# Optimization experiments

Hardware: AMD Instinct MI355X
Metric: run time of the kernel (lower is better)

Reference implementation:

```python
import jax, jax.numpy as jnp
import numpy as np

V = 4
H, W, Z = 32, 64, 13
C = 256
NH = 8
WS = (4, 4, 1)
SS = (2, 2, 0)
HID = 1024


def _layernorm(x, g, b):
    mu = jnp.mean(x, axis=-1, keepdims=True)
    var = jnp.mean((x - mu) ** 2, axis=-1, keepdims=True)
    return (x - mu) * jax.lax.rsqrt(var + 1e-5) * g + b


def setup_inputs() -> dict:
    key = jax.random.key(0)
    ks = jax.random.split(key, 12)
    B = 2
    s = 0.02
    return {
        "x_z": jax.random.normal(ks[0], (B, H, W, Z, C), jnp.float32),
        "x_q": jax.random.normal(ks[1], (B, H, W, Z, C), jnp.float32),
        "x_t": jax.random.normal(ks[2], (B, H, W, Z, C), jnp.float32),
        "x_u": jax.random.normal(ks[3], (B, H, W, Z, C), jnp.float32),
        "qkv_w": jax.random.normal(ks[4], (V, C, 3 * C), jnp.float32) * s,
        "qkv_b": jnp.zeros((V, 3 * C), jnp.float32),
        "proj_w": jax.random.normal(ks[5], (V, C, C), jnp.float32) * s,
        "proj_b": jnp.zeros((V, C), jnp.float32),
        "n1_g": jnp.ones((V, C), jnp.float32),
        "n1_b": jnp.zeros((V, C), jnp.float32),
        "n2_g": jnp.ones((V, C), jnp.float32),
        "n2_b": jnp.zeros((V, C), jnp.float32),
        "fc1_w": jax.random.normal(ks[6], (V, C, HID), jnp.float32) * s,
        "fc1_b": jnp.zeros((V, HID), jnp.float32),
        "fc2_w": jax.random.normal(ks[7], (V, HID, C), jnp.float32) * s,
        "fc2_b": jnp.zeros((V, C), jnp.float32),
    }


def reference(x_z, x_q, x_t, x_u, qkv_w, qkv_b, proj_w, proj_b,
              n1_g, n1_b, n2_g, n2_b, fc1_w, fc1_b, fc2_w, fc2_b):
    x = jnp.stack([x_z, x_q, x_t, x_u], axis=0)  # [V,B,H,W,Z,C]
    B = x.shape[1]
    L = H * W * Z
    w0, w1, w2 = WS
    N = w0 * w1 * w2
    hd = C // NH
    scale = hd ** -0.5

    shortcut = x.reshape(V, B, L, C)
    xn = _layernorm(shortcut, n1_g[:, None, None, :], n1_b[:, None, None, :])
    xs = xn.reshape(V, B, H, W, Z, C)
    # cyclic shift (same sign used for both rolls in the source)
    xs = jnp.roll(xs, shift=SS, axis=(2, 3, 4))
    # window partition -> [V, B_, N, C]
    xw = xs.reshape(V, B, H // w0, w0, W // w1, w1, Z // w2, w2, C)
    xw = xw.transpose(0, 1, 2, 4, 6, 3, 5, 7, 8).reshape(V, -1, N, C)
    B_ = xw.shape[1]

    qkv = jnp.einsum('vbnc,vcd->vbnd', xw, qkv_w) + qkv_b[:, None, None, :]
    qkv = qkv.reshape(V, B_, N, 3, NH, hd).transpose(3, 1, 0, 4, 2, 5)  # [3,B_,V,NH,N,hd]
    q, k, v = qkv[0], qkv[1], qkv[2]
    # per-(variable, head) attention: heads of different variables are concatenated
    attn = jax.nn.softmax(jnp.einsum('bvhnd,bvhmd->bvhnm', q * scale, k), axis=-1)
    ctx = jnp.einsum('bvhnm,bvhmd->bvhnd', attn, v)  # [B_,V,NH,N,hd]
    # faithful to torch reshape (B_, N, V*NH, hd) -> (B_, V*N, C): rows interleave (n, v)
    big = ctx.transpose(0, 3, 1, 2, 4).reshape(B_, V * N, C)
    y = big.reshape(B_, V, N, C).transpose(1, 0, 2, 3)  # slice [:, i*N:(i+1)*N]
    y = jnp.einsum('vbnc,vcd->vbnd', y, proj_w) + proj_b[:, None, None, :]
    # window reverse
    y = y.reshape(V, B, H // w0, W // w1, Z // w2, w0, w1, w2, C)
    y = y.transpose(0, 1, 2, 5, 3, 6, 4, 7, 8).reshape(V, B, H, W, Z, C)
    y = jnp.roll(y, shift=SS, axis=(2, 3, 4))  # same-sign roll (preserves source behavior)
    y = y.reshape(V, B, L, C)

    x2 = shortcut + y
    xm = _layernorm(x2, n2_g[:, None, None, :], n2_b[:, None, None, :])
    h = jax.nn.gelu(jnp.einsum('vblc,vcd->vbld', xm, fc1_w) + fc1_b[:, None, None, :],
                    approximate=False)
    m = jnp.einsum('vbld,vdc->vblc', h, fc2_w) + fc2_b[:, None, None, :]
    out = (x2 + m).reshape(V, B, H, W, Z, C)
    return out  # stacked per-variable outputs in variable_order
```

## Files before the change

kernel.cpp:

```cpp
#include <hip/hip_runtime.h>
#include <hip/hip_bf16.h>
#include <cstdint>
#include <cstddef>

#define DI __device__ __forceinline__

typedef __bf16 bf16_t;
typedef bf16_t bf16x8 __attribute__((ext_vector_type(8)));
typedef float f32x4 __attribute__((ext_vector_type(4)));

constexpr int Vn = 4, Bn = 2, Hn = 32, Wn = 64, Zn = 13, Cn = 256, HIDn = 1024;
constexpr int Ln = Hn * Wn * Zn;
constexpr int BWn = Bn * (Hn / 4) * (Wn / 4) * Zn;
constexpr int PB = Bn * Ln;
constexpr int ROWS = Vn * PB;

DI void gload_lds16(const void* g, void* l) {
  __builtin_amdgcn_global_load_lds(
      (const __attribute__((address_space(1))) void*)g,
      (__attribute__((address_space(3))) void*)l, 16, 0, 0);
}

DI unsigned short f2bf_bits(float f) {
  __hip_bfloat16 h = __float2bfloat16(f);
  return *reinterpret_cast<unsigned short*>(&h);
}

DI float gelu_f(float x) {
  float u = x * x;
  float w = x * fmaf(0.044715f, u, 1.0f);
  float e = __expf(-1.5957691216057308f * w);
  return x * __builtin_amdgcn_rcpf(1.0f + e);
}

__global__ __launch_bounds__(256) void transpose_tile_kernel(
    const float* __restrict__ src, __hip_bfloat16* __restrict__ dst, int K, int N) {
  __shared__ float S[64][65];
  const int n0 = blockIdx.x * 64, k0 = blockIdx.y * 64, v = blockIdx.z;
  const int tc = threadIdx.x & 63, tr = threadIdx.x >> 6;
#pragma unroll
  for (int i = 0; i < 16; ++i) {
    int kk = tr + i * 4;
    S[kk][tc] = src[((size_t)v * K + k0 + kk) * N + n0 + tc];
  }
  __syncthreads();
#pragma unroll
  for (int i = 0; i < 16; ++i) {
    int nn = tr + i * 4;
    dst[((size_t)v * N + n0 + nn) * K + k0 + tc] = __float2bfloat16(S[tc][nn]);
  }
}

__global__ __launch_bounds__(256) void ln1_kernel(
    const float* __restrict__ x0, const float* __restrict__ x1,
    const float* __restrict__ x2i, const float* __restrict__ x3,
    const float* __restrict__ g_, const float* __restrict__ b_,
    __hip_bfloat16* __restrict__ xw) {
  int gw = blockIdx.x * 4 + (threadIdx.x >> 6);
  int lane = threadIdx.x & 63;
  int v = gw / PB;
  int rem = gw - v * PB;
  int bw = rem >> 4, nn = rem & 15;
  int zb = bw % 13;
  int t = bw / 13;
  int wb = t & 15, t2 = t >> 4;
  int hb = t2 & 7, b = t2 >> 3;
  int hs = (hb * 4 + (nn >> 2) + 30) & 31;
  int wsrc = (wb * 4 + (nn & 3) + 62) & 63;
  size_t l = (size_t)(hs * 64 + wsrc) * 13 + zb;
  const float* xv = (v == 0) ? x0 : (v == 1) ? x1 : (v == 2) ? x2i : x3;
  const float* xp = xv + ((size_t)b * Ln + l) * 256;
  float4 val = *(const float4*)(xp + lane * 4);
  float s = val.x + val.y + val.z + val.w;
  float sq = val.x * val.x + val.y * val.y + val.z * val.z + val.w * val.w;
#pragma unroll
  for (int o = 32; o; o >>= 1) {
    s += __shfl_xor(s, o);
    sq += __shfl_xor(sq, o);
  }
  float mean = s * (1.0f / 256.0f);
  float var = sq * (1.0f / 256.0f) - mean * mean;
  float rstd = rsqrtf(var + 1e-5f);
  const float* gg = g_ + v * 256 + lane * 4;
  const float* bb = b_ + v * 256 + lane * 4;
  ushort4 o4;
  o4.x = f2bf_bits((val.x - mean) * rstd * gg[0] + bb[0]);
  o4.y = f2bf_bits((val.y - mean) * rstd * gg[1] + bb[1]);
  o4.z = f2bf_bits((val.z - mean) * rstd * gg[2] + bb[2]);
  o4.w = f2bf_bits((val.w - mean) * rstd * gg[3] + bb[3]);
  *reinterpret_cast<ushort4*>(xw + (size_t)gw * 256 + lane * 4) = o4;
}

__global__ __launch_bounds__(256) void attn_kernel(
    const __hip_bfloat16* __restrict__ qkvp, __hip_bfloat16* __restrict__ ctx) {
  __shared__ float P[4][16][17];
  int b_ = blockIdx.x;
  int v = blockIdx.y;
  int wid = threadIdx.x >> 6, lane = threadIdx.x & 63;
  int lm = lane & 15, hi = lane >> 4;
  const bf16_t* base = (const bf16_t*)qkvp + (size_t)(v * BWn + b_) * 16 * 768;
  const float scale = 0.17677669529663687f;
  f32x4 zero = {0.f, 0.f, 0.f, 0.f};
#pragma unroll
  for (int hh = 0; hh < 2; ++hh) {
    int h = wid + 4 * hh;
    bf16x8 qf = *(const bf16x8*)(base + (size_t)lm * 768 + h * 32 + hi * 8);
    bf16x8 kf = *(const bf16x8*)(base + (size_t)lm * 768 + 256 + h * 32 + hi * 8);
    f32x4 s = __builtin_amdgcn_mfma_f32_16x16x32_bf16(qf, kf, zero, 0, 0, 0);
    float p0[4];
#pragma unroll
    for (int q = 0; q < 4; ++q) {
      float val = s[q] * scale;
      float mx = val;
#pragma unroll
      for (int o = 8; o >= 1; o >>= 1) mx = fmaxf(mx, __shfl_xor(mx, o));
      float e = __expf(val - mx);
      float sum = e;
#pragma unroll
      for (int o = 8; o >= 1; o >>= 1) sum += __shfl_xor(sum, o);
      p0[q] = e * __builtin_amdgcn_rcpf(sum);
    }
#pragma unroll
    for (int q = 0; q < 4; ++q) P[wid][hi * 4 + q][lm] = p0[q];
    bf16x8 pa;
#pragma unroll
    for (int j = 0; j < 8; ++j) pa[j] = (bf16_t)0.f;
    if (hi < 2) {
#pragma unroll
      for (int j = 0; j < 8; ++j) pa[j] = (bf16_t)P[wid][lm][hi * 8 + j];
    }
#pragma unroll
    for (int dh = 0; dh < 2; ++dh) {
      bf16x8 vf;
#pragma unroll
      for (int j = 0; j < 8; ++j) vf[j] = (bf16_t)0.f;
      if (hi < 2) {
#pragma unroll
        for (int j = 0; j < 8; ++j)
          vf[j] = base[(size_t)(hi * 8 + j) * 768 + 512 + h * 32 + dh * 16 + lm];
      }
      f32x4 c = __builtin_amdgcn_mfma_f32_16x16x32_bf16(pa, vf, zero, 0, 0, 0);
#pragma unroll
      for (int q = 0; q < 4; ++q) {
        int n = hi * 4 + q;
        int d = dh * 16 + lm;
        int r = n * 4 + v;
        int vo = r >> 4, no = r & 15;
        ctx[((size_t)(vo * BWn + b_) * 16 + no) * 256 + h * 32 + d] = __float2bfloat16(c[q]);
      }
    }
  }
}

template <int EPI, int K, int N>
__global__ __launch_bounds__(256, 3) void gemm4(
    const __hip_bfloat16* __restrict__ A, const __hip_bfloat16* __restrict__ WT,
    const float* __restrict__ bias, __hip_bfloat16* __restrict__ outb,
    float* __restrict__ outf, const float* __restrict__ xi0,
    const float* __restrict__ xi1, const float* __restrict__ xi2,
    const float* __restrict__ xi3) {
  constexpr int NT = K / 64;
  constexpr int NC = N / 128;
  const int v = blockIdx.z;
  const int x = blockIdx.x;
  const int xcd = x & 7;
  const int j = x >> 3;
  const int c = j % NC;
  const int r = xcd + 8 * (j / NC);
  const int rowBase = r * 128;
  const int colBase = c * 128;

  const bf16_t* Av = (const bf16_t*)A + ((size_t)v * PB + rowBase) * K;
  const bf16_t* Wv = (const bf16_t*)WT + ((size_t)v * N + colBase) * K;

  __shared__ __align__(16) uint8_t smem[40960];
  bf16_t(*As)[64] = (bf16_t(*)[64])smem;
  bf16_t(*Bs)[64] = (bf16_t(*)[64])(smem + 16384);

  const int tid = threadIdx.x, wid = tid >> 6, lane = tid & 63;
  const int wr = wid >> 1, wc = wid & 1;
  const int lm = lane & 15, hi = lane >> 4;
  const int rA = lane >> 3;
  const int lg = (lane & 7) ^ rA;

  f32x4 acc[4][4];
#pragma unroll
  for (int m = 0; m < 4; ++m)
#pragma unroll
    for (int n = 0; n < 4; ++n) acc[m][n] = f32x4{0.f, 0.f, 0.f, 0.f};

  for (int t = 0; t < NT; ++t) {
    if (t) __syncthreads();
#pragma unroll
    for (int g = 0; g < 4; ++g) {
      int grp = wid * 4 + g;
      gload_lds16(Av + (size_t)(grp * 8 + rA) * K + t * 64 + lg * 8, &As[grp * 8][0]);
    }
#pragma unroll
    for (int g = 0; g < 4; ++g) {
      int grp = wid * 4 + g;
      gload_lds16(Wv + (size_t)(grp * 8 + rA) * K + t * 64 + lg * 8, &Bs[grp * 8][0]);
    }
    __syncthreads();
#pragma unroll
    for (int kk = 0; kk < 2; ++kk) {
      bf16x8 af[4], bfv[4];
#pragma unroll
      for (int m = 0; m < 4; ++m) {
        const int rr = wr * 64 + m * 16 + lm;
        af[m] = *(const bf16x8*)&As[rr][((kk * 4 + hi) ^ (lm & 7)) * 8];
      }
#pragma unroll
      for (int n = 0; n < 4; ++n) {
        const int rr = wc * 64 + n * 16 + lm;
        bfv[n] = *(const bf16x8*)&Bs[rr][((kk * 4 + hi) ^ (lm & 7)) * 8];
      }
#pragma unroll
      for (int m = 0; m < 4; ++m)
#pragma unroll
        for (int n = 0; n < 4; ++n)
          acc[m][n] = __builtin_amdgcn_mfma_f32_16x16x32_bf16(af[m], bfv[n], acc[m][n], 0, 0, 0);
    }
  }

  __syncthreads();
  uint8_t* ep = smem + wid * 10240;

  if constexpr (EPI == 0) {
    ushort(*E)[72] = (ushort(*)[72])ep;
    float bcol[4];
#pragma unroll
    for (int n = 0; n < 4; ++n) bcol[n] = bias[v * N + colBase + wc * 64 + n * 16 + lm];
#pragma unroll
    for (int m = 0; m < 4; ++m)
#pragma unroll
      for (int q = 0; q < 4; ++q) {
        int lr = m * 16 + hi * 4 + q;
#pragma unroll
        for (int n = 0; n < 4; ++n) E[lr][n * 16 + lm] = f2bf_bits(acc[m][n][q] + bcol[n]);
      }
    const int pr = lane >> 3, pc = lane & 7;
#pragma unroll
    for (int p = 0; p < 8; ++p) {
      int lr = p * 8 + pr;
      bf16x8 val = *(const bf16x8*)&E[lr][pc * 8];
      size_t grow = (size_t)v * PB + rowBase + wr * 64 + lr;
      int gcol = colBase + wc * 64 + pc * 8;
      *(bf16x8*)&outb[grow * N + gcol] = val;
    }
  } else {
    float(*F)[36] = (float(*)[36])ep;
    const int pr = lane >> 3, pc = lane & 7;
#pragma unroll
    for (int h2 = 0; h2 < 2; ++h2) {
#pragma unroll
      for (int m = 0; m < 4; ++m)
#pragma unroll
        for (int q = 0; q < 4; ++q) {
          int lr = m * 16 + hi * 4 + q;
#pragma unroll
          for (int n2 = 0; n2 < 2; ++n2) F[lr][n2 * 16 + lm] = acc[m][h2 * 2 + n2][q];
        }
#pragma unroll
      for (int p = 0; p < 8; ++p) {
        int lr = p * 8 + pr;
        f32x4 a4 = *(const f32x4*)&F[lr][pc * 4];
        int rowv = rowBase + wr * 64 + lr;
        int gcol = colBase + wc * 64 + h2 * 32 + pc * 4;
        f32x4 b4 = *(const f32x4*)&bias[v * N + gcol];
        int b_ = rowv >> 4, nn = rowv & 15;
        int zb = b_ % 13;
        int tt = b_ / 13;
        int wb = tt & 15, tt2 = tt >> 4;
        int hb = tt2 & 7, bb = tt2 >> 3;
        int h2v = (hb * 4 + (nn >> 2) + 2) & 31;
        int w2v = (wb * 4 + (nn & 3) + 2) & 63;
        size_t l = (size_t)(h2v * 64 + w2v) * 13 + zb;
        const float* xv = (v == 0) ? xi0 : (v == 1) ? xi1 : (v == 2) ? xi2 : xi3;
        f32x4 x4 = *(const f32x4*)(xv + ((size_t)bb * Ln + l) * 256 + gcol);
        f32x4 o4 = a4 + b4 + x4;
        *(f32x4*)(outf + (((size_t)v * Bn + bb) * Ln + l) * 256 + gcol) = o4;
      }
      if (h2 == 0) __builtin_amdgcn_s_waitcnt(0);
    }
  }
}

__global__ __launch_bounds__(512, 4) void mlp_fused6(
    const float* __restrict__ x2,
    const __hip_bfloat16* __restrict__ W1T,
    const __hip_bfloat16* __restrict__ W2T,
    const float* __restrict__ b1, const float* __restrict__ b2,
    const float* __restrict__ g2, const float* __restrict__ bt2,
    float* __restrict__ outp) {
  const int v = blockIdx.z;
  const size_t gRow0 = (size_t)v * PB + (size_t)blockIdx.x * 128;

  __shared__ __align__(16) uint8_t smem[73728];
  uint8_t* hb = smem + 65536;

  const int tid = threadIdx.x, wid = tid >> 6, lane = tid & 63;
  const int lm = lane & 15, hi = lane >> 4;
  const int rA = lane >> 3, lg = (lane & 7) ^ rA;

  {
    f32x4 g4 = *(const f32x4*)(g2 + v * 256 + lane * 4);
    f32x4 b4l = *(const f32x4*)(bt2 + v * 256 + lane * 4);
    for (int i = 0; i < 16; ++i) {
      int r = wid * 16 + i;
      const float* xp = x2 + (gRow0 + r) * 256;
      float4 val = *(const float4*)(xp + lane * 4);
      float s = val.x + val.y + val.z + val.w;
      float sq = val.x * val.x + val.y * val.y + val.z * val.z + val.w * val.w;
#pragma unroll
      for (int o = 32; o; o >>= 1) {
        s += __shfl_xor(s, o);
        sq += __shfl_xor(sq, o);
      }
      float mean = s * (1.0f / 256.0f);
      float var = sq * (1.0f / 256.0f) - mean * mean;
      float rstd = rsqrtf(var + 1e-5f);
      ushort4 o4;
      o4.x = f2bf_bits((val.x - mean) * rstd * g4[0] + b4l[0]);
      o4.y = f2bf_bits((val.y - mean) * rstd * g4[1] + b4l[1]);
      o4.z = f2bf_bits((val.z - mean) * rstd * g4[2] + b4l[2]);
      o4.w = f2bf_bits((val.w - mean) * rstd * g4[3] + b4l[3]);
      int gph = ((lm >> 1) ^ (r & 7) ^ hi) & 7;
      *(ushort4*)(smem + hi * 16384 + r * 128 + gph * 16 + (lm & 1) * 8) = o4;
    }
  }
  __syncthreads();

  bf16x8 xnf[4][2];
  {
    int r = wid * 16 + lm;
#pragma unroll
    for (int t = 0; t < 4; ++t)
#pragma unroll
      for (int kk = 0; kk < 2; ++kk) {
        int gph = ((kk * 4 + hi) ^ (r & 7) ^ t) & 7;
        xnf[t][kk] = *(const bf16x8*)(smem + t * 16384 + r * 128 + gph * 16);
      }
  }

  f32x4 acc2[16];
#pragma unroll
  for (int ca = 0; ca < 16; ++ca) acc2[ca] = f32x4{0.f, 0.f, 0.f, 0.f};

  const bf16_t* W1v = (const bf16_t*)W1T + (size_t)v * 1024 * 256;
  const bf16_t* W2v = (const bf16_t*)W2T + (size_t)v * 256 * 1024;

  auto stageW = [&](uint8_t* W1c, uint8_t* W2c, int hc) {
#pragma unroll
    for (int s = 0; s < 2; ++s) {
      int idx = wid * 2 + s;
      int t = idx >> 2, grp = idx & 3;
      gload_lds16(W1v + (size_t)(hc * 32 + grp * 8 + rA) * 256 + t * 64 + lg * 8,
                  W1c + t * 4096 + grp * 1024);
    }
#pragma unroll
    for (int s = 0; s < 2; ++s) {
      int i = wid * 2 + s;
      int p = i * 8 + rA;
      int col = 2 * p + (lg >> 2);
      gload_lds16(W2v + (size_t)col * 1024 + hc * 32 + (lg & 3) * 8, W2c + i * 1024);
    }
  };

  __syncthreads();
  stageW(smem, smem + 16384, 0);
  __syncthreads();

  for (int hc = 0; hc < 32; ++hc) {
    const int cur = hc & 1;
    uint8_t* W1c = smem + (cur ? 32768 : 0);
    uint8_t* W2c = smem + (cur ? 49152 : 16384);
    if (hc + 1 < 32)
      stageW(smem + (cur ? 0 : 32768), smem + (cur ? 16384 : 49152), hc + 1);

    int xr = wid * 16 + lm;
    int p = xr >> 1;
#pragma unroll
    for (int t2 = 0; t2 < 2; ++t2) {
      f32x4 acc1 = f32x4{0.f, 0.f, 0.f, 0.f};
      int hw = t2 * 16 + lm;
#pragma unroll
      for (int t = 0; t < 4; ++t)
#pragma unroll
        for (int kk = 0; kk < 2; ++kk) {
          bf16x8 w1f = *(const bf16x8*)(W1c + t * 4096 + hw * 128 +
                                        (((kk * 4 + hi) ^ (hw & 7)) & 7) * 16);
          acc1 = __builtin_amdgcn_mfma_f32_16x16x32_bf16(w1f, xnf[t][kk], acc1, 0, 0, 0);
        }
      f32x4 b1v = *(const f32x4*)&b1[v * 1024 + hc * 32 + t2 * 16 + hi * 4];
      ushort4 hp;
      hp.x = f2bf_bits(gelu_f(acc1[0] + b1v[0]));
      hp.y = f2bf_bits(gelu_f(acc1[1] + b1v[1]));
      hp.z = f2bf_bits(gelu_f(acc1[2] + b1v[2]));
      hp.w = f2bf_bits(gelu_f(acc1[3] + b1v[3]));
      int glog = (xr & 1) * 4 + t2 * 2 + (hi >> 1);
      int gph = (glog ^ (p & 7)) & 7;
      *(ushort4*)(hb + p * 128 + gph * 16 + (hi & 1) * 8) = hp;
    }
    __syncthreads();

    {
      bf16x8 hf = *(const bf16x8*)(hb + p * 128 + ((((xr & 1) * 4 + hi) ^ (p & 7)) & 7) * 16);
#pragma unroll
      for (int ca = 0; ca < 16; ++ca) {
        int col = ca * 16 + lm;
        int p2 = col >> 1;
        bf16x8 w2f = *(const bf16x8*)(W2c + p2 * 128 +
                                      ((((col & 1) * 4 + hi) ^ (p2 & 7)) & 7) * 16);
        acc2[ca] = __builtin_amdgcn_mfma_f32_16x16x32_bf16(w2f, hf, acc2[ca], 0, 0, 0);
      }
    }
    __syncthreads();
  }

  {
    size_t orow = gRow0 + wid * 16 + lm;
    float* obase = outp + orow * 256;
#pragma unroll
    for (int ca = 0; ca < 16; ++ca) {
      int col = ca * 16 + hi * 4;
      f32x4 b4 = *(const f32x4*)&b2[v * 256 + col];
      float* o = obase + col;
      f32x4 cur = *(const f32x4*)o;
      f32x4 res = cur + acc2[ca] + b4;
      *(f32x4*)o = res;
    }
  }
}

extern "C" void kernel_launch(void* const* d_in, const int* in_sizes, int n_in,
                              void* d_out, int out_size, void* d_ws, size_t ws_size,
                              hipStream_t stream) {
  const float* x0 = (const float*)d_in[0];
  const float* x1 = (const float*)d_in[1];
  const float* x2i = (const float*)d_in[2];
  const float* x3 = (const float*)d_in[3];
  const float* qkv_w = (const float*)d_in[4];
  const float* qkv_b = (const float*)d_in[5];
  const float* proj_w = (const float*)d_in[6];
  const float* proj_b = (const float*)d_in[7];
  const float* n1g = (const float*)d_in[8];
  const float* n1b = (const float*)d_in[9];
  const float* n2g = (const float*)d_in[10];
  const float* n2b = (const float*)d_in[11];
  const float* fc1_w = (const float*)d_in[12];
  const float* fc1_b = (const float*)d_in[13];
  const float* fc2_w = (const float*)d_in[14];
  const float* fc2_b = (const float*)d_in[15];
  float* out = (float*)d_out;

  uint8_t* ws = (uint8_t*)d_ws;
  size_t off = 0;
  auto alloc = [&](size_t bytes) -> void* {
    void* p = ws + off;
    off += (bytes + 255) & ~(size_t)255;
    return p;
  };
  __hip_bfloat16* wqkvT = (__hip_bfloat16*)alloc((size_t)Vn * Cn * 768 * 2);
  __hip_bfloat16* wprojT = (__hip_bfloat16*)alloc((size_t)Vn * Cn * Cn * 2);
  __hip_bfloat16* wfc1T = (__hip_bfloat16*)alloc((size_t)Vn * Cn * HIDn * 2);
  __hip_bfloat16* wfc2T = (__hip_bfloat16*)alloc((size_t)Vn * HIDn * Cn * 2);
  __hip_bfloat16* xw = (__hip_bfloat16*)alloc((size_t)ROWS * Cn * 2);
  __hip_bfloat16* qkvb = (__hip_bfloat16*)alloc((size_t)ROWS * 768 * 2);

  transpose_tile_kernel<<<dim3(768 / 64, 256 / 64, Vn), 256, 0, stream>>>(qkv_w, wqkvT, 256, 768);
  transpose_tile_kernel<<<dim3(256 / 64, 256 / 64, Vn), 256, 0, stream>>>(proj_w, wprojT, 256, 256);
  transpose_tile_kernel<<<dim3(1024 / 64, 256 / 64, Vn), 256, 0, stream>>>(fc1_w, wfc1T, 256, 1024);
  transpose_tile_kernel<<<dim3(256 / 64, 1024 / 64, Vn), 256, 0, stream>>>(fc2_w, wfc2T, 1024, 256);

  ln1_kernel<<<ROWS / 4, 256, 0, stream>>>(x0, x1, x2i, x3, n1g, n1b, xw);

  gemm4<0, 256, 768><<<dim3(416 * 6, 1, Vn), 256, 0, stream>>>(
      xw, wqkvT, qkv_b, qkvb, nullptr, nullptr, nullptr, nullptr, nullptr);

  attn_kernel<<<dim3(BWn, Vn), 256, 0, stream>>>(qkvb, xw );

  gemm4<1, 256, 256><<<dim3(416 * 2, 1, Vn), 256, 0, stream>>>(
      xw , wprojT, proj_b, nullptr, out , x0, x1, x2i, x3);

  mlp_fused6<<<dim3(PB / 128, 1, Vn), 512, 0, stream>>>(
      out , wfc1T, wfc2T, fc1_b, fc2_b, n2g, n2b, out);
}
```

Before: 908.1 us.

## Shrink MLP tile to 64 rows, pass hidden activations via bpermute, drop double buffering

The fused MLP kernel now processes 64 rows per block with 256 threads instead of 128 rows with 512. It drops the LDS round-trip for the GELU hidden tile and moves the fc1 accumulator layout into the fc2 operand layout with ds_bpermute in registers. It also removes the double-buffered weight staging, which cuts LDS to 32KB so more blocks can be resident. The trade-off is twice as many weight loads per row and no overlap between weight staging and compute within a block.

```diff
diff --git a/kernel.cpp b/kernel.cpp
--- a/kernel.cpp
+++ b/kernel.cpp
@@ -286,7 +286,7 @@
   }
 }
 
-__global__ __launch_bounds__(512, 4) void mlp_fused6(
+__global__ __launch_bounds__(256, 4) void mlp_fused9(
     const float* __restrict__ x2,
     const __hip_bfloat16* __restrict__ W1T,
     const __hip_bfloat16* __restrict__ W2T,
@@ -294,10 +294,11 @@
     const float* __restrict__ g2, const float* __restrict__ bt2,
     float* __restrict__ outp) {
   const int v = blockIdx.z;
-  const size_t gRow0 = (size_t)v * PB + (size_t)blockIdx.x * 128;
-
-  __shared__ __align__(16) uint8_t smem[73728];
-  uint8_t* hb = smem + 65536;
+  const size_t gRow0 = (size_t)v * PB + (size_t)blockIdx.x * 64;
+
+  __shared__ __align__(16) uint8_t smem[32768];
+  uint8_t* W1c = smem;
+  uint8_t* W2c = smem + 16384;
 
   const int tid = threadIdx.x, wid = tid >> 6, lane = tid & 63;
   const int lm = lane & 15, hi = lane >> 4;
@@ -326,7 +327,7 @@
       o4.z = f2bf_bits((val.z - mean) * rstd * g4[2] + b4l[2]);
       o4.w = f2bf_bits((val.w - mean) * rstd * g4[3] + b4l[3]);
       int gph = ((lm >> 1) ^ (r & 7) ^ hi) & 7;
-      *(ushort4*)(smem + hi * 16384 + r * 128 + gph * 16 + (lm & 1) * 8) = o4;
+      *(ushort4*)(smem + hi * 8192 + r * 128 + gph * 16 + (lm & 1) * 8) = o4;
     }
   }
   __syncthreads();
@@ -339,9 +340,15 @@
 #pragma unroll
       for (int kk = 0; kk < 2; ++kk) {
         int gph = ((kk * 4 + hi) ^ (r & 7) ^ t) & 7;
-        xnf[t][kk] = *(const bf16x8*)(smem + t * 16384 + r * 128 + gph * 16);
-      }
-  }
+        xnf[t][kk] = *(const bf16x8*)(smem + t * 8192 + r * 128 + gph * 16);
+      }
+  }
+
+  const int base_w1_k0 = lm * 128 + ((((0 * 4) + hi) ^ (lm & 7)) & 7) * 16;
+  const int base_w1_k1 = lm * 128 + ((((1 * 4) + hi) ^ (lm & 7)) & 7) * 16;
+  const int base_w2 = (lm >> 1) * 128 + ((((lm & 1) * 4 + hi) ^ ((lm >> 1) & 7)) & 7) * 16;
+  const int addrA = (2 * (hi & 1) * 16 + lm) * 4;
+  const int addrB = addrA + 64;
 
   f32x4 acc2[16];
 #pragma unroll
@@ -350,70 +357,70 @@
   const bf16_t* W1v = (const bf16_t*)W1T + (size_t)v * 1024 * 256;
   const bf16_t* W2v = (const bf16_t*)W2T + (size_t)v * 256 * 1024;
 
-  auto stageW = [&](uint8_t* W1c, uint8_t* W2c, int hc) {
-#pragma unroll
-    for (int s = 0; s < 2; ++s) {
-      int idx = wid * 2 + s;
+  __syncthreads();
+
+  for (int hc = 0; hc < 32; ++hc) {
+#pragma unroll
+    for (int s = 0; s < 4; ++s) {
+      int idx = wid * 4 + s;
       int t = idx >> 2, grp = idx & 3;
       gload_lds16(W1v + (size_t)(hc * 32 + grp * 8 + rA) * 256 + t * 64 + lg * 8,
                   W1c + t * 4096 + grp * 1024);
     }
 #pragma unroll
-    for (int s = 0; s < 2; ++s) {
-      int i = wid * 2 + s;
+    for (int s = 0; s < 4; ++s) {
+      int i = wid * 4 + s;
       int p = i * 8 + rA;
       int col = 2 * p + (lg >> 2);
       gload_lds16(W2v + (size_t)col * 1024 + hc * 32 + (lg & 3) * 8, W2c + i * 1024);
     }
-  };
-
-  __syncthreads();
-  stageW(smem, smem + 16384, 0);
-  __syncthreads();
-
-  for (int hc = 0; hc < 32; ++hc) {
-    const int cur = hc & 1;
-    uint8_t* W1c = smem + (cur ? 32768 : 0);
-    uint8_t* W2c = smem + (cur ? 49152 : 16384);
-    if (hc + 1 < 32)
-      stageW(smem + (cur ? 0 : 32768), smem + (cur ? 16384 : 49152), hc + 1);
-
-    int xr = wid * 16 + lm;
-    int p = xr >> 1;
+    __syncthreads();
+
+    f32x4 acc1[2];
+    acc1[0] = f32x4{0.f, 0.f, 0.f, 0.f};
+    acc1[1] = f32x4{0.f, 0.f, 0.f, 0.f};
+#pragma unroll
+    for (int t2 = 0; t2 < 2; ++t2)
+#pragma unroll
+      for (int t = 0; t < 4; ++t)
+#pragma unroll
+        for (int kk = 0; kk < 2; ++kk) {
+          const int off = t * 4096 + t2 * 2048 + (kk ? base_w1_k1 : base_w1_k0);
+          bf16x8 w1f = *(const bf16x8*)(W1c + off);
+          acc1[t2] = __builtin_amdgcn_mfma_f32_16x16x32_bf16(w1f, xnf[t][kk], acc1[t2], 0, 0, 0);
+        }
+
+    uint32_t P0[2], P1[2];
 #pragma unroll
     for (int t2 = 0; t2 < 2; ++t2) {
-      f32x4 acc1 = f32x4{0.f, 0.f, 0.f, 0.f};
-      int hw = t2 * 16 + lm;
-#pragma unroll
-      for (int t = 0; t < 4; ++t)
-#pragma unroll
-        for (int kk = 0; kk < 2; ++kk) {
-          bf16x8 w1f = *(const bf16x8*)(W1c + t * 4096 + hw * 128 +
-                                        (((kk * 4 + hi) ^ (hw & 7)) & 7) * 16);
-          acc1 = __builtin_amdgcn_mfma_f32_16x16x32_bf16(w1f, xnf[t][kk], acc1, 0, 0, 0);
-        }
       f32x4 b1v = *(const f32x4*)&b1[v * 1024 + hc * 32 + t2 * 16 + hi * 4];
-      ushort4 hp;
-      hp.x = f2bf_bits(gelu_f(acc1[0] + b1v[0]));
-      hp.y = f2bf_bits(gelu_f(acc1[1] + b1v[1]));
-      hp.z = f2bf_bits(gelu_f(acc1[2] + b1v[2]));
-      hp.w = f2bf_bits(gelu_f(acc1[3] + b1v[3]));
-      int glog = (xr & 1) * 4 + t2 * 2 + (hi >> 1);
-      int gph = (glog ^ (p & 7)) & 7;
-      *(ushort4*)(hb + p * 128 + gph * 16 + (hi & 1) * 8) = hp;
-    }
-    __syncthreads();
-
-    {
-      bf16x8 hf = *(const bf16x8*)(hb + p * 128 + ((((xr & 1) * 4 + hi) ^ (p & 7)) & 7) * 16);
-#pragma unroll
-      for (int ca = 0; ca < 16; ++ca) {
-        int col = ca * 16 + lm;
-        int p2 = col >> 1;
-        bf16x8 w2f = *(const bf16x8*)(W2c + p2 * 128 +
-                                      ((((col & 1) * 4 + hi) ^ (p2 & 7)) & 7) * 16);
-        acc2[ca] = __builtin_amdgcn_mfma_f32_16x16x32_bf16(w2f, hf, acc2[ca], 0, 0, 0);
-      }
+      unsigned short e0 = f2bf_bits(gelu_f(acc1[t2][0] + b1v[0]));
+      unsigned short e1 = f2bf_bits(gelu_f(acc1[t2][1] + b1v[1]));
+      unsigned short e2 = f2bf_bits(gelu_f(acc1[t2][2] + b1v[2]));
+      unsigned short e3 = f2bf_bits(gelu_f(acc1[t2][3] + b1v[3]));
+      P0[t2] = (uint32_t)e0 | ((uint32_t)e1 << 16);
+      P1[t2] = (uint32_t)e2 | ((uint32_t)e3 << 16);
+    }
+
+    uint32_t a0A = __builtin_amdgcn_ds_bpermute(addrA, (int)P0[0]);
+    uint32_t a1A = __builtin_amdgcn_ds_bpermute(addrA, (int)P0[1]);
+    uint32_t b0A = __builtin_amdgcn_ds_bpermute(addrA, (int)P1[0]);
+    uint32_t b1A = __builtin_amdgcn_ds_bpermute(addrA, (int)P1[1]);
+    uint32_t a0B = __builtin_amdgcn_ds_bpermute(addrB, (int)P0[0]);
+    uint32_t a1B = __builtin_amdgcn_ds_bpermute(addrB, (int)P0[1]);
+    uint32_t b0B = __builtin_amdgcn_ds_bpermute(addrB, (int)P1[0]);
+    uint32_t b1B = __builtin_amdgcn_ds_bpermute(addrB, (int)P1[1]);
+    uint4 hw4;
+    hw4.x = (hi < 2) ? a0A : a1A;
+    hw4.y = (hi < 2) ? b0A : b1A;
+    hw4.z = (hi < 2) ? a0B : a1B;
+    hw4.w = (hi < 2) ? b0B : b1B;
+    bf16x8 hf = *reinterpret_cast<bf16x8*>(&hw4);
+
+#pragma unroll
+    for (int ca = 0; ca < 16; ++ca) {
+      bf16x8 w2f = *(const bf16x8*)(W2c + ca * 1024 + base_w2);
+      acc2[ca] = __builtin_amdgcn_mfma_f32_16x16x32_bf16(w2f, hf, acc2[ca], 0, 0, 0);
     }
     __syncthreads();
   }
@@ -483,6 +490,6 @@
   gemm4<1, 256, 256><<<dim3(416 * 2, 1, Vn), 256, 0, stream>>>(
       xw , wprojT, proj_b, nullptr, out , x0, x1, x2i, x3);
 
-  mlp_fused6<<<dim3(PB / 128, 1, Vn), 512, 0, stream>>>(
+  mlp_fused9<<<dim3(PB / 64, 1, Vn), 256, 0, stream>>>(
       out , wfc1T, wfc2T, fc1_b, fc2_b, n2g, n2b, out);
 }
```

Result: slower. 947.1 us (+4.3%).
